# Performance work log

Hardware: AMD Instinct MI355X
Metric: run time of the kernel (lower is better)

The kernel has to match this reference:

```python
import jax, jax.numpy as jnp
import numpy as np

K = 20      # neighbors per node
D_T = 32    # timestep embedding dim

def _timestep_embedding(t, dim):
    half = dim // 2
    freqs = jnp.exp(-jnp.log(10000.0) * jnp.arange(half, dtype=jnp.float32) / (half - 1))
    args = t[:, None] * freqs[None, :]
    return jnp.concatenate([jnp.sin(args), jnp.cos(args)], axis=-1)

def _knn(pos, k):
    # pos: [N,3] -> (sources, targets): [N*k] edge index lists
    r2 = jnp.sum(pos * pos, axis=-1)
    d2 = r2[:, None] + r2[None, :] - 2.0 * (pos @ pos.T)   # [N,N] squared distances
    n = pos.shape[0]
    d2 = d2 + 1e10 * jnp.eye(n, dtype=pos.dtype)           # exclude self
    d2 = jax.lax.stop_gradient(d2)                         # indices only, no grad path
    _, idx = jax.lax.top_k(-d2, k)                         # [N,k]
    targets = jnp.repeat(jnp.arange(n), k)
    sources = idx.reshape(-1)
    return sources, targets

def _forward(z, t, conditioning, Wc1, bc1, Wc2, bc2, Wc3, bc3, We1, be1, We2, be2, Wn1, bn1, Wn2, bn2, alpha, beta):
    B, N, _ = z.shape
    pos, vel, massf = z[..., :3], z[..., 3:6], z[..., 6:]
    t = t * jnp.ones((B,), z.dtype)
    temb = _timestep_embedding(t, D_T)                     # [B,32]
    cond = jnp.concatenate([temb, conditioning], axis=1)   # [B,36]
    h = jax.nn.gelu(cond @ Wc1 + bc1)
    h = jax.nn.gelu(h @ Wc2 + bc2)
    cond = h @ Wc3 + bc3                                   # [B,36]
    fs = massf + cond[:, None, :]                          # scalar node feats [B,N,36]

    def single(pos_b, vel_b, fs_b):
        src, tgt = _knn(pos_b, K)
        rel = pos_b[src] - pos_b[tgt]                      # [E,3]
        r2 = jnp.sum(rel * rel, axis=-1, keepdims=True)
        vs, vt = vel_b[src], vel_b[tgt]
        # rotation-invariant edge features
        inv = jnp.concatenate([
            fs_b[src], fs_b[tgt], r2,
            jnp.sum(vs * vt, -1, keepdims=True),
            jnp.sum(vs * rel, -1, keepdims=True),
            jnp.sum(vt * rel, -1, keepdims=True),
        ], axis=-1)                                        # [E,76]
        e = jax.nn.gelu(inv @ We1 + be1) @ We2 + be2       # [E,4]
        logit, smsg, c_rel, c_vel = e[:, 0], e[:, 1], e[:, 2], e[:, 3]
        # segment softmax over incoming edges of each target node
        m = jax.ops.segment_max(logit, tgt, num_segments=N)
        a = jnp.exp(logit - m[tgt])
        denom = jax.ops.segment_sum(a, tgt, num_segments=N)
        w = a / denom[tgt]
        # equivariant vector messages, invariant scalar messages
        vmsg = w[:, None] * (c_rel[:, None] * rel + c_vel[:, None] * vs)
        vagg = jax.ops.segment_sum(vmsg, tgt, num_segments=N)              # [N,3]
        sagg = jax.ops.segment_sum(w * smsg, tgt, num_segments=N)[:, None]  # [N,1]
        hn = jax.nn.gelu(jnp.concatenate([fs_b, sagg], axis=-1) @ Wn1 + bn1)
        sout = hn @ Wn2 + bn2                              # [N,1] 0e output
        pos_out = pos_b + alpha * vagg                     # 1o
        feat_out = jnp.concatenate([beta * vagg, sout], axis=-1)  # 1o + 0e
        return jnp.concatenate([pos_out, feat_out], axis=-1)      # [N,7]

    h_all = jax.vmap(single)(pos, vel, fs)
    return z + h_all

def setup_inputs():
    key = jax.random.key(0)
    ks = jax.random.split(key, 10)
    B, N = 2, 8192
    d_cond = D_T + 4          # 36
    e_in = 2 * d_cond + 4     # 76
    e_hid, n_hid = 128, 64
    g = lambda i, shp: jax.random.normal(ks[i], shp, jnp.float32) * 0.05
    return {
        "z": jax.random.normal(ks[0], (B, N, 7), jnp.float32),
        "t": jax.random.uniform(ks[1], (B,), jnp.float32),
        "conditioning": jax.random.normal(ks[2], (B, 4), jnp.float32),
        "mask": jnp.ones((B, N), dtype=bool),
        "Wc1": g(3, (d_cond, 4 * d_cond)), "bc1": jnp.zeros((4 * d_cond,), jnp.float32),
        "Wc2": g(4, (4 * d_cond, 4 * d_cond)), "bc2": jnp.zeros((4 * d_cond,), jnp.float32),
        "Wc3": g(5, (4 * d_cond, d_cond)), "bc3": jnp.zeros((d_cond,), jnp.float32),
        "We1": g(6, (e_in, e_hid)), "be1": jnp.zeros((e_hid,), jnp.float32),
        "We2": g(7, (e_hid, 4)), "be2": jnp.zeros((4,), jnp.float32),
        "Wn1": g(8, (d_cond + 1, n_hid)), "bn1": jnp.zeros((n_hid,), jnp.float32),
        "Wn2": g(9, (n_hid, 1)), "bn2": jnp.zeros((1,), jnp.float32),
        "alpha": jnp.float32(0.1), "beta": jnp.float32(0.1),
    }

def reference(z, t, conditioning, mask, Wc1, bc1, Wc2, bc2, Wc3, bc3, We1, be1, We2, be2, Wn1, bn1, Wn2, bn2, alpha, beta):
    # mask is unused (module docstring: does not support masking)
    return _forward(z, t, conditioning, Wc1, bc1, Wc2, bc2, Wc3, bc3, We1, be1, We2, be2, Wn1, bn1, Wn2, bn2, alpha, beta)
```

## Files before the change

kernel.cpp:

```cpp
#include <hip/hip_runtime.h>
#include <math.h>

#define NB 8192
#define BATCH 2
#define KNN 20
#define BN (BATCH*NB)
#define NE (BN*KNN)
#define GT 16
#define NG 8

__device__ __forceinline__ float gelu_f(float x){
    float x3 = x*x*x;
    float a = 0.7978845608028654f*(x + 0.044715f*x3);
    float e2 = __expf(2.0f*a);
    float th = 1.0f - 2.0f/(e2+1.0f);
    return 0.5f*x*(1.0f+th);
}

__device__ __forceinline__ float wave_sum(float v){
    #pragma unroll
    for (int s=1;s<64;s<<=1) v += __shfl_xor(v, s);
    return v;
}
__device__ __forceinline__ float wave_max(float v){
    #pragma unroll
    for (int s=1;s<64;s<<=1) v = fmaxf(v, __shfl_xor(v, s));
    return v;
}

__global__ __launch_bounds__(256) void prep_kernel(const float* __restrict__ z,
                                                   float4* __restrict__ pos4,
                                                   float4* __restrict__ vel4){
    int g = blockIdx.x*256 + threadIdx.x;
    if (g >= BN) return;
    const float* zp = z + (size_t)g*7;
    float x = zp[0], y = zp[1], zz = zp[2];
    float r2 = x*x + y*y + zz*zz;
    pos4[g] = make_float4(x, y, zz, r2);
    vel4[g] = make_float4(zp[3], zp[4], zp[5], zp[6]);
}

__global__ __launch_bounds__(256) void cond_kernel(const float* __restrict__ t,
        const float* __restrict__ conditioning,
        const float* __restrict__ Wc1, const float* __restrict__ bc1,
        const float* __restrict__ Wc2, const float* __restrict__ bc2,
        const float* __restrict__ Wc3, const float* __restrict__ bc3,
        const float* __restrict__ We1, const float* __restrict__ be1,
        const float* __restrict__ We2,
        const float* __restrict__ Wn1, const float* __restrict__ bn1,
        float* __restrict__ consts, float* __restrict__ pack){
    int b = blockIdx.x;
    int tid = threadIdx.x;
    __shared__ float ci[36];
    __shared__ float h1[144];
    __shared__ float h2[144];
    __shared__ float cnd[36];
    float tv = t[b];
    if (tid < 16){
        float f = expf(-9.210340371976184f * (float)tid / 15.0f);
        float a = tv*f;
        ci[tid]    = sinf(a);
        ci[16+tid] = cosf(a);
    }
    if (tid < 4) ci[32+tid] = conditioning[b*4+tid];
    __syncthreads();
    if (tid < 144){
        float acc = bc1[tid];
        #pragma unroll
        for (int c=0;c<36;c++) acc += ci[c]*Wc1[c*144+tid];
        h1[tid] = gelu_f(acc);
    }
    __syncthreads();
    if (tid < 144){
        float acc = bc2[tid];
        #pragma unroll 36
        for (int c=0;c<144;c++) acc += h1[c]*Wc2[c*144+tid];
        h2[tid] = gelu_f(acc);
    }
    __syncthreads();
    if (tid < 36){
        float acc = bc3[tid];
        #pragma unroll 36
        for (int c=0;c<144;c++) acc += h2[c]*Wc3[c*36+tid];
        cnd[tid] = acc;
    }
    __syncthreads();
    if (tid < 128){
        float accC = be1[tid], s1 = 0.f, s2 = 0.f;
        #pragma unroll
        for (int c=0;c<36;c++){
            float w1 = We1[c*128+tid];
            float w2 = We1[(36+c)*128+tid];
            accC += cnd[c]*(w1+w2);
            s1 += w1; s2 += w2;
        }
        consts[b*128+tid] = accC;
        pack[tid*12 + b] = accC;
        if (b==0){
            consts[256+tid] = s1; consts[384+tid] = s2;
            pack[tid*12+2] = s1;
            pack[tid*12+3] = s2;
            pack[tid*12+4] = We1[72*128+tid];
            pack[tid*12+5] = We1[73*128+tid];
            pack[tid*12+6] = We1[74*128+tid];
            pack[tid*12+7] = We1[75*128+tid];
            pack[tid*12+8]  = We2[tid*4+0];
            pack[tid*12+9]  = We2[tid*4+1];
            pack[tid*12+10] = We2[tid*4+2];
            pack[tid*12+11] = We2[tid*4+3];
        }
    }
    if (tid < 64){
        float accD = bn1[tid], t1 = 0.f;
        #pragma unroll
        for (int c=0;c<36;c++){
            float w = Wn1[c*64+tid];
            accD += cnd[c]*w;
            t1 += w;
        }
        consts[512 + b*64 + tid] = accD;
        if (b==0) consts[640+tid] = t1;
    }
}

__global__ __launch_bounds__(512, 4) void knn_kernel(const float4* __restrict__ pos4,
                                                     int* __restrict__ nbr){
    __shared__ float4 sPos[GT*64];
    __shared__ float2 sCand[32*64];
    int tid = threadIdx.x;
    int w = tid >> 6, lane = tid & 63;
    int n0g = blockIdx.x * 32;
    int b = n0g >> 13;
    int n0 = n0g & (NB-1);
    const float4* __restrict__ P = pos4 + b*NB;

    int nw = n0 + w*4;
    float nx[4], ny[4], nz[4], pw[4], acc[4];
    #pragma unroll
    for (int k=0;k<4;k++){
        float4 p = P[nw+k];
        nx[k] = -2.0f*p.x; ny[k] = -2.0f*p.y; nz[k] = -2.0f*p.z; pw[k] = p.w;
        acc[k] = 3.0e38f;
    }
    int selfTile = n0 >> 6;
    int sl0 = (n0 & 63) + w*4;

    float4 pre0 = P[(w*2    )*64 + lane];
    float4 pre1 = P[(w*2 + 1)*64 + lane];
    for (int g=0; g<NG; ++g){
        __syncthreads();
        sPos[(w*2    )*64 + lane] = pre0;
        sPos[(w*2 + 1)*64 + lane] = pre1;
        if (g+1 < NG){
            pre0 = P[((g+1)*GT + w*2    )*64 + lane];
            pre1 = P[((g+1)*GT + w*2 + 1)*64 + lane];
        }
        __syncthreads();
        int tbase = g*GT;
        #pragma unroll
        for (int t=0;t<GT;t++){
            float4 q = sPos[t*64 + lane];
            if (tbase + t != selfTile){
                #pragma unroll
                for (int k=0;k<4;k++){
                    float d2 = fmaf(nx[k],q.x, fmaf(ny[k],q.y, fmaf(nz[k],q.z, pw[k]+q.w)));
                    acc[k] = fminf(acc[k], d2);
                }
            } else {
                #pragma unroll
                for (int k=0;k<4;k++){
                    float d2 = fmaf(nx[k],q.x, fmaf(ny[k],q.y, fmaf(nz[k],q.z, pw[k]+q.w)));
                    if (lane == sl0 + k) d2 = 3.0e38f;
                    acc[k] = fminf(acc[k], d2);
                }
            }
        }
    }

    float T[4];
    #pragma unroll
    for (int k=0;k<4;k++){
        float v = acc[k];
        #pragma unroll
        for (int K=2; K<=64; K<<=1){
            #pragma unroll
            for (int j=K>>1; j>0; j>>=1){
                float o = __shfl_xor(v, j);
                bool keepmin = (((lane & j) == 0) == ((lane & K) == 0));
                float mn = fminf(v,o), mx = fmaxf(v,o);
                v = keepmin ? mn : mx;
            }
        }
        T[k] = __shfl(v, 19);
    }

    int cnt[4];
    #pragma unroll
    for (int k=0;k<4;k++) cnt[k] = 0;
    unsigned long long lt = (1ull << lane) - 1ull;

    pre0 = P[(w*2    )*64 + lane];
    pre1 = P[(w*2 + 1)*64 + lane];
    for (int g=0; g<NG; ++g){
        __syncthreads();
        sPos[(w*2    )*64 + lane] = pre0;
        sPos[(w*2 + 1)*64 + lane] = pre1;
        if (g+1 < NG){
            pre0 = P[((g+1)*GT + w*2    )*64 + lane];
            pre1 = P[((g+1)*GT + w*2 + 1)*64 + lane];
        }
        __syncthreads();
        int tbase = g*GT;
        #pragma unroll 4
        for (int t=0;t<GT;t++){
            int tile = tbase + t;
            float4 q = sPos[t*64 + lane];
            int j = (tile<<6) + lane;
            bool selft = (tile == selfTile);
            #pragma unroll
            for (int k=0;k<4;k++){
                float d2 = fmaf(nx[k],q.x, fmaf(ny[k],q.y, fmaf(nz[k],q.z, pw[k]+q.w)));
                bool hit = (d2 <= T[k]);
                if (selft && (lane == sl0 + k)) hit = false;
                unsigned long long m = __ballot(hit);
                if (m){
                    if (hit){
                        int off = cnt[k] + (int)__popcll(m & lt);
                        if (off < 64)
                            sCand[(w*4+k)*64 + off] = make_float2(d2, __int_as_float(j));
                    }
                    cnt[k] += (int)__popcll(m);
                }
            }
        }
    }

    #pragma unroll
    for (int k=0;k<4;k++){
        int m = cnt[k]; if (m > 64) m = 64;
        float d; int idx;
        if (lane < m){
            float2 e = sCand[(w*4+k)*64 + lane];
            d = e.x; idx = __float_as_int(e.y);
        } else { d = 3.0e38f; idx = 0x7f000000 + lane; }
        #pragma unroll
        for (int K=2; K<=64; K<<=1){
            #pragma unroll
            for (int j=K>>1; j>0; j>>=1){
                float od = __shfl_xor(d, j);
                int   oi = __shfl_xor(idx, j);
                bool pless = (od < d) || (od == d && oi < idx);
                bool keepmin = (((lane & j) == 0) == ((lane & K) == 0));
                if (pless == keepmin){ d = od; idx = oi; }
            }
        }
        if (lane < KNN) nbr[(size_t)(n0g + w*4 + k)*KNN + lane] = idx;
    }
}

__global__ __launch_bounds__(256) void edge_kernel(const float4* __restrict__ pos4,
        const float4* __restrict__ vel4,
        const int* __restrict__ nbr,
        const float* __restrict__ pack,
        const float* __restrict__ be2,
        float* __restrict__ ebuf){
    int tid = threadIdx.x;
    bool bb = (blockIdx.x >= (NE/2/256));

    int e = blockIdx.x*256 + tid;
    int i = e / KNN;
    int b = i >> 13;
    int s = nbr[e];
    float4 ps = pos4[b*NB + s];
    float4 pt = pos4[i];
    float4 vs = vel4[b*NB + s];
    float4 vt = vel4[i];
    float rx = ps.x - pt.x, ry = ps.y - pt.y, rz = ps.z - pt.z;
    float r2  = rx*rx + ry*ry + rz*rz;
    float vv  = vs.x*vt.x + vs.y*vt.y + vs.z*vt.z;
    float vsr = vs.x*rx + vs.y*ry + vs.z*rz;
    float vtr = vt.x*rx + vt.y*ry + vt.z*rz;
    float mfs = vs.w, mft = vt.w;

    float e0 = be2[0], e1 = be2[1], e2v = be2[2], e3 = be2[3];
    #pragma unroll 8
    for (int h=0; h<128; h++){
        const float4* pb = (const float4*)(pack + h*12);
        float4 A = pb[0];
        float4 Bv = pb[1];
        float4 C = pb[2];
        float base = bb ? A.y : A.x;
        float x = base + mfs*A.z + mft*A.w + r2*Bv.x + vv*Bv.y + vsr*Bv.z + vtr*Bv.w;
        float gx = gelu_f(x);
        e0  += gx*C.x;
        e1  += gx*C.y;
        e2v += gx*C.z;
        e3  += gx*C.w;
    }
    ebuf[e]        = e0;
    ebuf[NE + e]   = e1;
    ebuf[2*NE + e] = e2v*rx + e3*vs.x;
    ebuf[3*NE + e] = e2v*ry + e3*vs.y;
    ebuf[4*NE + e] = e2v*rz + e3*vs.z;
}

__global__ __launch_bounds__(256) void node_kernel(const float* __restrict__ z,
        const float4* __restrict__ vel4,
        const float* __restrict__ consts,
        const float* __restrict__ Wn1,
        const float* __restrict__ Wn2,
        const float* __restrict__ bn2,
        const float* __restrict__ alpha_p,
        const float* __restrict__ beta_p,
        const float* __restrict__ ebuf,
        float* __restrict__ out){
    int g = blockIdx.x*4 + (threadIdx.x>>6);
    int lane = threadIdx.x & 63;
    int b = g >> 13;

    float lg = -3.0e38f, sm = 0.f, ux = 0.f, uy = 0.f, uz = 0.f;
    if (lane < KNN){
        size_t e = (size_t)g*KNN + lane;
        lg = ebuf[e]; sm = ebuf[NE+e]; ux = ebuf[2*NE+e]; uy = ebuf[3*NE+e]; uz = ebuf[4*NE+e];
    }
    float mx = wave_max(lg);
    float a = (lane < KNN) ? __expf(lg - mx) : 0.0f;
    float denom = wave_sum(a);
    float wv = a / denom;
    float sagg = wave_sum(wv*sm);
    float vax  = wave_sum(wv*ux);
    float vay  = wave_sum(wv*uy);
    float vaz  = wave_sum(wv*uz);

    float mf = vel4[g].w;
    float x = consts[512 + b*64 + lane] + mf*consts[640+lane] + sagg*Wn1[36*64+lane];
    float y = gelu_f(x)*Wn2[lane];
    float sout = wave_sum(y) + bn2[0];

    if (lane < 7){
        float alpha = alpha_p[0], beta = beta_p[0];
        float zl = z[(size_t)g*7 + lane];
        float r;
        if      (lane==0) r = zl + alpha*vax;
        else if (lane==1) r = zl + alpha*vay;
        else if (lane==2) r = zl + alpha*vaz;
        else if (lane==3) r = beta*vax;
        else if (lane==4) r = beta*vay;
        else if (lane==5) r = beta*vaz;
        else              r = sout;
        out[(size_t)g*7 + lane] = zl + r;
    }
}

extern "C" void kernel_launch(void* const* d_in, const int* in_sizes, int n_in,
                              void* d_out, int out_size, void* d_ws, size_t ws_size,
                              hipStream_t stream) {
    const float* z    = (const float*)d_in[0];
    const float* t    = (const float*)d_in[1];
    const float* cond = (const float*)d_in[2];
    const float* Wc1  = (const float*)d_in[4];
    const float* bc1  = (const float*)d_in[5];
    const float* Wc2  = (const float*)d_in[6];
    const float* bc2  = (const float*)d_in[7];
    const float* Wc3  = (const float*)d_in[8];
    const float* bc3  = (const float*)d_in[9];
    const float* We1  = (const float*)d_in[10];
    const float* be1  = (const float*)d_in[11];
    const float* We2  = (const float*)d_in[12];
    const float* be2  = (const float*)d_in[13];
    const float* Wn1  = (const float*)d_in[14];
    const float* bn1  = (const float*)d_in[15];
    const float* Wn2  = (const float*)d_in[16];
    const float* bn2  = (const float*)d_in[17];
    const float* alp  = (const float*)d_in[18];
    const float* bet  = (const float*)d_in[19];
    float* out = (float*)d_out;

    char* ws = (char*)d_ws;
    float4* pos4   = (float4*)(ws);
    float4* vel4   = (float4*)(ws + 262144);
    float*  consts = (float*)(ws + 524288);
    float*  pack   = (float*)(ws + 528384);
    int*    nbr    = (int*)(ws + 534528);
    float*  ebuf   = (float*)(ws + 1845248);

    prep_kernel<<<dim3(BN/256), dim3(256), 0, stream>>>(z, pos4, vel4);
    cond_kernel<<<dim3(BATCH), dim3(256), 0, stream>>>(t, cond, Wc1, bc1, Wc2, bc2,
                                                       Wc3, bc3, We1, be1, We2, Wn1, bn1,
                                                       consts, pack);
    knn_kernel<<<dim3(BN/32), dim3(512), 0, stream>>>(pos4, nbr);
    edge_kernel<<<dim3(NE/256), dim3(256), 0, stream>>>(pos4, vel4, nbr, pack, be2, ebuf);
    node_kernel<<<dim3(BN/4), dim3(256), 0, stream>>>(z, vel4, consts, Wn1, Wn2, bn2,
                                                      alp, bet, ebuf, out);
}
```

Baseline: 217.7 us.

## Fuse edge and node kernels via shared memory; merge prep with cond kernel

Merges the edge MLP and the per-node softmax aggregation into one kernel. Each 320-thread block handles 16 nodes with 20 edges each, so the edge results stay in shared memory instead of making a round trip through a global buffer. The edge MLP weights are staged in shared memory rather than read from global each iteration, and the prep and cond kernels are combined to save a launch. The softmax reduction now runs serially on 16 threads per block, and gelu uses a fast divide.

After: 208.5 us (median of 2 runs). 4.2% less time.

```diff
diff --git a/kernel.cpp b/kernel.cpp
--- a/kernel.cpp
+++ b/kernel.cpp
@@ -8,39 +8,18 @@
 #define NE (BN*KNN)
 #define GT 16
 #define NG 8
+#define BIG 3.0e38f
 
 __device__ __forceinline__ float gelu_f(float x){
     float x3 = x*x*x;
     float a = 0.7978845608028654f*(x + 0.044715f*x3);
     float e2 = __expf(2.0f*a);
-    float th = 1.0f - 2.0f/(e2+1.0f);
+    float th = 1.0f - __fdividef(2.0f, e2+1.0f);
     return 0.5f*x*(1.0f+th);
 }
 
-__device__ __forceinline__ float wave_sum(float v){
-    #pragma unroll
-    for (int s=1;s<64;s<<=1) v += __shfl_xor(v, s);
-    return v;
-}
-__device__ __forceinline__ float wave_max(float v){
-    #pragma unroll
-    for (int s=1;s<64;s<<=1) v = fmaxf(v, __shfl_xor(v, s));
-    return v;
-}
-
-__global__ __launch_bounds__(256) void prep_kernel(const float* __restrict__ z,
-                                                   float4* __restrict__ pos4,
-                                                   float4* __restrict__ vel4){
-    int g = blockIdx.x*256 + threadIdx.x;
-    if (g >= BN) return;
-    const float* zp = z + (size_t)g*7;
-    float x = zp[0], y = zp[1], zz = zp[2];
-    float r2 = x*x + y*y + zz*zz;
-    pos4[g] = make_float4(x, y, zz, r2);
-    vel4[g] = make_float4(zp[3], zp[4], zp[5], zp[6]);
-}
-
-__global__ __launch_bounds__(256) void cond_kernel(const float* __restrict__ t,
+__global__ __launch_bounds__(256) void prepcond_kernel(const float* __restrict__ z,
+        const float* __restrict__ t,
         const float* __restrict__ conditioning,
         const float* __restrict__ Wc1, const float* __restrict__ bc1,
         const float* __restrict__ Wc2, const float* __restrict__ bc2,
@@ -48,9 +27,18 @@
         const float* __restrict__ We1, const float* __restrict__ be1,
         const float* __restrict__ We2,
         const float* __restrict__ Wn1, const float* __restrict__ bn1,
+        float4* __restrict__ pos4, float4* __restrict__ vel4,
         float* __restrict__ consts, float* __restrict__ pack){
+    int tid = threadIdx.x;
+    int g = blockIdx.x*256 + tid;
+    const float* zp = z + (size_t)g*7;
+    float x = zp[0], y = zp[1], zz = zp[2];
+    float r2 = x*x + y*y + zz*zz;
+    pos4[g] = make_float4(x, y, zz, r2);
+    vel4[g] = make_float4(zp[3], zp[4], zp[5], zp[6]);
+
+    if (blockIdx.x >= BATCH) return;
     int b = blockIdx.x;
-    int tid = threadIdx.x;
     __shared__ float ci[36];
     __shared__ float h1[144];
     __shared__ float h2[144];
@@ -140,7 +128,7 @@
     for (int k=0;k<4;k++){
         float4 p = P[nw+k];
         nx[k] = -2.0f*p.x; ny[k] = -2.0f*p.y; nz[k] = -2.0f*p.z; pw[k] = p.w;
-        acc[k] = 3.0e38f;
+        acc[k] = BIG;
     }
     int selfTile = n0 >> 6;
     int sl0 = (n0 & 63) + w*4;
@@ -170,7 +158,7 @@
                 #pragma unroll
                 for (int k=0;k<4;k++){
                     float d2 = fmaf(nx[k],q.x, fmaf(ny[k],q.y, fmaf(nz[k],q.z, pw[k]+q.w)));
-                    if (lane == sl0 + k) d2 = 3.0e38f;
+                    if (lane == sl0 + k) d2 = BIG;
                     acc[k] = fminf(acc[k], d2);
                 }
             }
@@ -242,7 +230,7 @@
         if (lane < m){
             float2 e = sCand[(w*4+k)*64 + lane];
             d = e.x; idx = __float_as_int(e.y);
-        } else { d = 3.0e38f; idx = 0x7f000000 + lane; }
+        } else { d = BIG; idx = 0x7f000000 + lane; }
         #pragma unroll
         for (int K=2; K<=64; K<<=1){
             #pragma unroll
@@ -258,97 +246,121 @@
     }
 }
 
-__global__ __launch_bounds__(256) void edge_kernel(const float4* __restrict__ pos4,
+__global__ __launch_bounds__(320) void edgenode_kernel(const float4* __restrict__ pos4,
         const float4* __restrict__ vel4,
         const int* __restrict__ nbr,
         const float* __restrict__ pack,
+        const float* __restrict__ consts,
+        const float* __restrict__ Wn1,
+        const float* __restrict__ Wn2,
         const float* __restrict__ be2,
-        float* __restrict__ ebuf){
+        const float* __restrict__ bn2,
+        const float* __restrict__ alpha_p,
+        const float* __restrict__ beta_p,
+        const float* __restrict__ z,
+        float* __restrict__ out){
+    __shared__ float4 sP[384];
+    __shared__ float sLg[320], sSm[320], sUx[320], sUy[320], sUz[320];
+    __shared__ float sD[64], sT1[64], sW36[64], sWo[64];
+    __shared__ float sMf[16];
+    __shared__ float4 sAgg[16];
+    __shared__ float sPart[320];
+
     int tid = threadIdx.x;
-    bool bb = (blockIdx.x >= (NE/2/256));
-
-    int e = blockIdx.x*256 + tid;
+    bool bb = (blockIdx.x >= 512);
+    for (int k=tid; k<384; k+=320) sP[k] = ((const float4*)pack)[k];
+    if (tid < 64){
+        sD[tid]   = consts[512 + (bb?64:0) + tid];
+        sT1[tid]  = consts[640+tid];
+        sW36[tid] = Wn1[36*64+tid];
+        sWo[tid]  = Wn2[tid];
+    }
+
+    int e = blockIdx.x*320 + tid;
     int i = e / KNN;
-    int b = i >> 13;
+    int ln = tid / KNN;
+    int r  = tid - ln*KNN;
+    int bbase = bb ? NB : 0;
     int s = nbr[e];
-    float4 ps = pos4[b*NB + s];
-    float4 pt = pos4[i];
-    float4 vs = vel4[b*NB + s];
-    float4 vt = vel4[i];
+    float4 ps = pos4[bbase + s], pt = pos4[i];
+    float4 vs = vel4[bbase + s], vt = vel4[i];
+    if (r == 0) sMf[ln] = vt.w;
+
     float rx = ps.x - pt.x, ry = ps.y - pt.y, rz = ps.z - pt.z;
     float r2  = rx*rx + ry*ry + rz*rz;
     float vv  = vs.x*vt.x + vs.y*vt.y + vs.z*vt.z;
     float vsr = vs.x*rx + vs.y*ry + vs.z*rz;
     float vtr = vt.x*rx + vt.y*ry + vt.z*rz;
     float mfs = vs.w, mft = vt.w;
-
-    float e0 = be2[0], e1 = be2[1], e2v = be2[2], e3 = be2[3];
-    #pragma unroll 8
+    __syncthreads();
+
+    float a0 = be2[0], a1 = be2[1], a2 = be2[2], a3 = be2[3];
+    #pragma unroll 4
     for (int h=0; h<128; h++){
-        const float4* pb = (const float4*)(pack + h*12);
-        float4 A = pb[0];
-        float4 Bv = pb[1];
-        float4 C = pb[2];
+        float4 A  = sP[h*3];
+        float4 Bv = sP[h*3+1];
+        float4 C  = sP[h*3+2];
         float base = bb ? A.y : A.x;
         float x = base + mfs*A.z + mft*A.w + r2*Bv.x + vv*Bv.y + vsr*Bv.z + vtr*Bv.w;
         float gx = gelu_f(x);
-        e0  += gx*C.x;
-        e1  += gx*C.y;
-        e2v += gx*C.z;
-        e3  += gx*C.w;
-    }
-    ebuf[e]        = e0;
-    ebuf[NE + e]   = e1;
-    ebuf[2*NE + e] = e2v*rx + e3*vs.x;
-    ebuf[3*NE + e] = e2v*ry + e3*vs.y;
-    ebuf[4*NE + e] = e2v*rz + e3*vs.z;
-}
-
-__global__ __launch_bounds__(256) void node_kernel(const float* __restrict__ z,
-        const float4* __restrict__ vel4,
-        const float* __restrict__ consts,
-        const float* __restrict__ Wn1,
-        const float* __restrict__ Wn2,
-        const float* __restrict__ bn2,
-        const float* __restrict__ alpha_p,
-        const float* __restrict__ beta_p,
-        const float* __restrict__ ebuf,
-        float* __restrict__ out){
-    int g = blockIdx.x*4 + (threadIdx.x>>6);
-    int lane = threadIdx.x & 63;
-    int b = g >> 13;
-
-    float lg = -3.0e38f, sm = 0.f, ux = 0.f, uy = 0.f, uz = 0.f;
-    if (lane < KNN){
-        size_t e = (size_t)g*KNN + lane;
-        lg = ebuf[e]; sm = ebuf[NE+e]; ux = ebuf[2*NE+e]; uy = ebuf[3*NE+e]; uz = ebuf[4*NE+e];
-    }
-    float mx = wave_max(lg);
-    float a = (lane < KNN) ? __expf(lg - mx) : 0.0f;
-    float denom = wave_sum(a);
-    float wv = a / denom;
-    float sagg = wave_sum(wv*sm);
-    float vax  = wave_sum(wv*ux);
-    float vay  = wave_sum(wv*uy);
-    float vaz  = wave_sum(wv*uz);
-
-    float mf = vel4[g].w;
-    float x = consts[512 + b*64 + lane] + mf*consts[640+lane] + sagg*Wn1[36*64+lane];
-    float y = gelu_f(x)*Wn2[lane];
-    float sout = wave_sum(y) + bn2[0];
-
-    if (lane < 7){
+        a0 += gx*C.x; a1 += gx*C.y; a2 += gx*C.z; a3 += gx*C.w;
+    }
+    sLg[tid] = a0;
+    sSm[tid] = a1;
+    sUx[tid] = a2*rx + a3*vs.x;
+    sUy[tid] = a2*ry + a3*vs.y;
+    sUz[tid] = a2*rz + a3*vs.z;
+    __syncthreads();
+
+    if (tid < 16){
+        int base = tid*KNN;
+        float m = -BIG;
+        #pragma unroll
+        for (int q=0;q<KNN;q++) m = fmaxf(m, sLg[base+q]);
+        float den=0.f, wx=0.f, wy=0.f, wz=0.f, wsm=0.f;
+        #pragma unroll
+        for (int q=0;q<KNN;q++){
+            float a = __expf(sLg[base+q]-m);
+            den += a;
+            wsm += a*sSm[base+q];
+            wx  += a*sUx[base+q];
+            wy  += a*sUy[base+q];
+            wz  += a*sUz[base+q];
+        }
+        float inv = __fdividef(1.0f, den);
+        sAgg[tid] = make_float4(wx*inv, wy*inv, wz*inv, wsm*inv);
+    }
+    __syncthreads();
+
+    {
+        float mf = sMf[ln];
+        float sg = sAgg[ln].w;
+        float part = 0.f;
+        #pragma unroll
+        for (int h=r; h<64; h+=KNN){
+            float x = sD[h] + mf*sT1[h] + sg*sW36[h];
+            part += gelu_f(x)*sWo[h];
+        }
+        sPart[tid] = part;
+    }
+    __syncthreads();
+
+    if (tid < 16){
+        float sout = bn2[0];
+        #pragma unroll
+        for (int q=0;q<KNN;q++) sout += sPart[tid*KNN+q];
+        int node = blockIdx.x*16 + tid;
         float alpha = alpha_p[0], beta = beta_p[0];
-        float zl = z[(size_t)g*7 + lane];
-        float r;
-        if      (lane==0) r = zl + alpha*vax;
-        else if (lane==1) r = zl + alpha*vay;
-        else if (lane==2) r = zl + alpha*vaz;
-        else if (lane==3) r = beta*vax;
-        else if (lane==4) r = beta*vay;
-        else if (lane==5) r = beta*vaz;
-        else              r = sout;
-        out[(size_t)g*7 + lane] = zl + r;
+        float4 ag = sAgg[tid];
+        const float* zp = z + (size_t)node*7;
+        float* op = out + (size_t)node*7;
+        op[0] = zp[0]*2.0f + alpha*ag.x;
+        op[1] = zp[1]*2.0f + alpha*ag.y;
+        op[2] = zp[2]*2.0f + alpha*ag.z;
+        op[3] = zp[3] + beta*ag.x;
+        op[4] = zp[4] + beta*ag.y;
+        op[5] = zp[5] + beta*ag.z;
+        op[6] = zp[6] + sout;
     }
 }
 
@@ -382,14 +394,11 @@
     float*  consts = (float*)(ws + 524288);
     float*  pack   = (float*)(ws + 528384);
     int*    nbr    = (int*)(ws + 534528);
-    float*  ebuf   = (float*)(ws + 1845248);
-
-    prep_kernel<<<dim3(BN/256), dim3(256), 0, stream>>>(z, pos4, vel4);
-    cond_kernel<<<dim3(BATCH), dim3(256), 0, stream>>>(t, cond, Wc1, bc1, Wc2, bc2,
-                                                       Wc3, bc3, We1, be1, We2, Wn1, bn1,
-                                                       consts, pack);
+
+    prepcond_kernel<<<dim3(BN/256), dim3(256), 0, stream>>>(z, t, cond,
+        Wc1, bc1, Wc2, bc2, Wc3, bc3, We1, be1, We2, Wn1, bn1,
+        pos4, vel4, consts, pack);
     knn_kernel<<<dim3(BN/32), dim3(512), 0, stream>>>(pos4, nbr);
-    edge_kernel<<<dim3(NE/256), dim3(256), 0, stream>>>(pos4, vel4, nbr, pack, be2, ebuf);
-    node_kernel<<<dim3(BN/4), dim3(256), 0, stream>>>(z, vel4, consts, Wn1, Wn2, bn2,
-                                                      alp, bet, ebuf, out);
+    edgenode_kernel<<<dim3(BN/16), dim3(320), 0, stream>>>(pos4, vel4, nbr, pack, consts,
+        Wn1, Wn2, be2, bn2, alp, bet, z, out);
 }
```
